# Performance work log

Measured on AMD Instinct MI355X. Metric: run time of the kernel, lower is better.

The kernel has to match this reference:

```python
import jax, jax.numpy as jnp
import numpy as np

B, D, RES, NSLOTS, NITERS = 32, 256, 64, 8, 3
NTOK = RES * RES
SCALE = D ** -0.5
EPS = 1e-8
LN_EPS = 1e-5


def _ln(x, g, b, axes=(-1,)):
    m = x.mean(axes, keepdims=True)
    v = x.var(axes, keepdims=True)
    return (x - m) / jnp.sqrt(v + LN_EPS) * g + b


def _build_grid(res):
    xy = jnp.linspace(0.0, 1.0, res)
    xx, yy = jnp.meshgrid(xy, xy, indexing='ij')
    g = jnp.stack([xx, yy], axis=-1)[None]  # [1,res,res,2]
    return jnp.concatenate([g, 1.0 - g], axis=-1)  # [1,res,res,4]


GRID = _build_grid(RES)


def setup_inputs() -> dict:
    key = jax.random.key(0)
    ks = iter(jax.random.split(key, 48))
    w = lambda shp: 0.02 * jax.random.normal(next(ks), shp, jnp.float32)
    z = lambda shp: jnp.zeros(shp, jnp.float32)
    o = lambda shp: jnp.ones(shp, jnp.float32)
    return dict(
        x=jax.random.normal(next(ks), (B, D, RES, RES), jnp.float32),
        eps_noise=jax.random.normal(next(ks), (B, NSLOTS, D), jnp.float32),
        pos_w=w((4, D)), pos_b=z((D,)),
        enc_g=o((NTOK, D)), enc_b=z((NTOK, D)),
        fm_w1=w((D, D)), fm_b1=z((D,)), fm_w2=w((D, D)), fm_b2=z((D,)),
        in_g=o((D,)), in_b=z((D,)),
        q_w=w((D, D)), q_b=z((D,)),
        k_w=w((D, D)), k_b=z((D,)),
        v_w=w((D, D)), v_b=z((D,)),
        gru_wih=w((D, 3 * D)), gru_whh=w((D, 3 * D)), gru_bih=z((3 * D,)), gru_bhh=z((3 * D,)),
        pre_g=o((D,)), pre_b=z((D,)),
        st_w1=w((D, D)), st_b1=z((D,)), st_w2=w((D, D)), st_b2=z((D,)),
        slot_g=o((D,)), slot_b=z((D,)),
        slots_loc=w((1, D)),
        slots_logscale=jax.random.uniform(next(ks), (1, D), jnp.float32),
    )


def reference(x, eps_noise, pos_w, pos_b, enc_g, enc_b, fm_w1, fm_b1, fm_w2, fm_b2,
              in_g, in_b, q_w, q_b, k_w, k_b, v_w, v_b,
              gru_wih, gru_whh, gru_bih, gru_bhh, pre_g, pre_b,
              st_w1, st_b1, st_w2, st_b2, slot_g, slot_b, slots_loc, slots_logscale):
    # SoftPositionEmbed: x + Linear(grid) permuted to NCHW
    pos = GRID @ pos_w + pos_b                       # [1,res,res,D]
    h = x + jnp.transpose(pos, (0, 3, 1, 2))         # [B,D,res,res]
    tokens = h.reshape(B, D, NTOK).transpose(0, 2, 1)  # [B,NTOK,D]
    # encoder_norm: LayerNorm over [NTOK, D] jointly
    tokens = _ln(tokens, enc_g, enc_b, axes=(-2, -1))
    tokens = jax.nn.relu(tokens @ fm_w1 + fm_b1)
    tokens = jax.nn.relu(tokens @ fm_w2 + fm_b2)
    tokens = _ln(tokens, in_g, in_b)                 # norm_input
    k = tokens @ k_w + k_b                           # [B,NTOK,D]
    v = tokens @ v_w + v_b
    # stochastic initial slots (non-variational branch)
    slots = slots_loc[None] + jnp.exp(slots_logscale)[None] * eps_noise  # [B,S,D]
    for _ in range(NITERS):
        prev = slots
        s = _ln(slots, slot_g, slot_b)               # norm_slots
        q = s @ q_w + q_b
        dots = jnp.einsum('bid,bjd->bij', q, k) * SCALE  # [B,S,NTOK]
        attn = jax.nn.softmax(dots, axis=1) + EPS    # softmax over SLOT axis
        attn = attn / attn.sum(-1, keepdims=True)    # renormalize over tokens
        upd = jnp.einsum('bij,bjd->bid', attn, v)    # [B,S,D]
        # GRUCell(update, prev) — torch gate order r,z,n
        gi = upd @ gru_wih + gru_bih
        gh = prev @ gru_whh + gru_bhh
        ir, iz, inn = jnp.split(gi, 3, axis=-1)
        hr, hz, hn = jnp.split(gh, 3, axis=-1)
        r = jax.nn.sigmoid(ir + hr)
        zt = jax.nn.sigmoid(iz + hz)
        n = jnp.tanh(inn + r * hn)
        slots = (1.0 - zt) * n + zt * prev
        # residual MLP: slots += slot_transformation(norm_pre_ff(slots))
        ff = _ln(slots, pre_g, pre_b)
        ff = jax.nn.relu(ff @ st_w1 + st_b1)
        ff = jax.nn.relu(ff @ st_w2 + st_b2)
        slots = slots + ff
    return slots
```

## Files before the change

### kernel.cpp

```cpp
#include <hip/hip_runtime.h>
#include <hip/hip_bf16.h>

typedef __attribute__((ext_vector_type(8))) short short8;
typedef __attribute__((ext_vector_type(4))) float f32x4;

#define DEVI static __device__ __forceinline__

DEVI ushort f2bf(float f) {
  union { __hip_bfloat16 h; ushort u; } c; c.h = __float2bfloat16(f); return c.u;
}
DEVI float bf2f(ushort u) {
  union { __hip_bfloat16 h; ushort u; } c; c.u = u; return __bfloat162float(c.h);
}

DEVI void gload16(const ushort* g, ushort* l) {
  __builtin_amdgcn_global_load_lds(
      (const __attribute__((address_space(1))) void*)g,
      (__attribute__((address_space(3))) void*)l, 16, 0, 0);
}

DEVI void blk_reduce2(float& a, float& b) {
  #pragma unroll
  for (int m = 1; m < 64; m <<= 1) {
    a += __shfl_xor(a, m);
    b += __shfl_xor(b, m);
  }
  __shared__ float sc[8];
  int tid = threadIdx.x, w = tid >> 6;
  if ((tid & 63) == 0) { sc[w * 2] = a; sc[w * 2 + 1] = b; }
  __syncthreads();
  if (tid == 0) {
    sc[0] = sc[0] + sc[2] + sc[4] + sc[6];
    sc[1] = sc[1] + sc[3] + sc[5] + sc[7];
  }
  __syncthreads();
  a = sc[0]; b = sc[1];
  __syncthreads();
}

DEVI void red256_2(float& a, float& b, float* sc8) {
  int tid = threadIdx.x;
  #pragma unroll
  for (int m = 1; m < 64; m <<= 1) {
    a += __shfl_xor(a, m);
    b += __shfl_xor(b, m);
  }
  if (tid < 256 && (tid & 63) == 0) { sc8[(tid >> 6) * 2] = a; sc8[(tid >> 6) * 2 + 1] = b; }
  __syncthreads();
  a = sc8[0] + sc8[2] + sc8[4] + sc8[6];
  b = sc8[1] + sc8[3] + sc8[5] + sc8[7];
  __syncthreads();
}

__global__ void kw_kernel(const float* w0, const float* w1, const float* w2, const float* w3,
                          ushort* wT, float* bstats) {
  int widx = blockIdx.y;
  const float* src = (widx == 0) ? w0 : (widx == 1) ? w1 : (widx == 2) ? w2 : w3;
  ushort* dst = wT + (size_t)widx * 65536;
  int tile = blockIdx.x;
  int k0 = (tile >> 2) * 64, n0 = (tile & 3) * 64;
  __shared__ float t[64][65];
  int tid = threadIdx.x;
  int r = tid >> 2, c0 = (tid & 3) * 16;
  #pragma unroll
  for (int j = 0; j < 16; j += 4) {
    float4 v = *reinterpret_cast<const float4*>(src + (size_t)(k0 + r) * 256 + n0 + c0 + j);
    t[r][c0 + j + 0] = v.x; t[r][c0 + j + 1] = v.y;
    t[r][c0 + j + 2] = v.z; t[r][c0 + j + 3] = v.w;
  }
  __syncthreads();
  ushort buf[16];
  #pragma unroll
  for (int j = 0; j < 16; j++) buf[j] = f2bf(t[c0 + j][r]);
  size_t o = (size_t)(n0 + r) * 256 + k0 + c0;
  *reinterpret_cast<uint4*>(dst + o) = *reinterpret_cast<uint4*>(&buf[0]);
  *reinterpret_cast<uint4*>(dst + o + 8) = *reinterpret_cast<uint4*>(&buf[8]);
  if (blockIdx.x == 0 && blockIdx.y == 0 && tid < 64) bstats[tid] = 0.f;
}

__global__ void kw2_kernel(const float* wih, const float* whh, const float* w1,
                           const float* w2, const float* qw,
                           ushort* grup, ushort* w1b, ushort* w2b, ushort* qwb) {
  int d = blockIdx.x, c = threadIdx.x;
  ushort p6[6];
  p6[0] = f2bf(wih[(size_t)d * 768 + c]);
  p6[1] = f2bf(wih[(size_t)d * 768 + 256 + c]);
  p6[2] = f2bf(wih[(size_t)d * 768 + 512 + c]);
  p6[3] = f2bf(whh[(size_t)d * 768 + c]);
  p6[4] = f2bf(whh[(size_t)d * 768 + 256 + c]);
  p6[5] = f2bf(whh[(size_t)d * 768 + 512 + c]);
  size_t o = ((size_t)d * 256 + c) * 6;
  *reinterpret_cast<uint3*>(grup + o) = *reinterpret_cast<uint3*>(p6);
  int i = d * 256 + c;
  w1b[i] = f2bf(w1[i]);
  w2b[i] = f2bf(w2[i]);
  qwb[i] = f2bf(qw[i]);
}

__global__ void k1_stats(const float* x, const float* pos_w, const float* pos_b, float* bstats) {
  int b = blockIdx.y, blk = blockIdx.x, tid = threadIdx.x;
  const float* xb = x + (size_t)b * 1048576;
  float s = 0.f, sq = 0.f;
  for (int i = 0; i < 16; i++) {
    int e4 = blk * 4096 + i * 256 + tid;
    int e = e4 * 4;
    int d = e >> 12, t = e & 4095;
    int ii = t >> 6, j0 = t & 63;
    float xx = ii * (1.f / 63.f);
    float c0 = pos_w[512 + d] + pos_w[768 + d] + pos_b[d];
    float cx = pos_w[d] - pos_w[512 + d];
    float cy = pos_w[256 + d] - pos_w[768 + d];
    float4 v = reinterpret_cast<const float4*>(xb)[e4];
    float base = c0 + xx * cx;
    #pragma unroll
    for (int j = 0; j < 4; j++) {
      float yy = (j0 + j) * (1.f / 63.f);
      float h = (&v.x)[j] + base + yy * cy;
      s += h; sq += h * h;
    }
  }
  blk_reduce2(s, sq);
  if (tid == 0) {
    atomicAdd(&bstats[b * 2], s);
    atomicAdd(&bstats[b * 2 + 1], sq);
  }
}

__global__ void k2_tokens(const float* x, const float* pos_w, const float* pos_b,
                          const float* enc_g, const float* enc_b, const float* bstats,
                          ushort* t0) {
  int tcx = blockIdx.x;
  int dcx = blockIdx.y;
  int b = blockIdx.z;
  int tid = threadIdx.x;
  float mean = bstats[b * 2] * (1.f / 1048576.f);
  float var = bstats[b * 2 + 1] * (1.f / 1048576.f) - mean * mean;
  float rstd = rsqrtf(var + 1e-5f);
  __shared__ float tt[64][65];
  const float* xb = x + (size_t)b * 1048576;
  float xx = tcx * (1.f / 63.f);
  #pragma unroll
  for (int it = 0; it < 4; it++) {
    int idx = tid + it * 256;
    int dl = idx >> 4, f4 = idx & 15;
    int d = dcx * 64 + dl;
    float c0 = pos_w[512 + d] + pos_w[768 + d] + pos_b[d];
    float cx = pos_w[d] - pos_w[512 + d];
    float cy = pos_w[256 + d] - pos_w[768 + d];
    float4 v = *reinterpret_cast<const float4*>(xb + (size_t)d * 4096 + tcx * 64 + f4 * 4);
    float base = c0 + xx * cx;
    #pragma unroll
    for (int j = 0; j < 4; j++) {
      float yy = (f4 * 4 + j) * (1.f / 63.f);
      tt[f4 * 4 + j][dl] = (&v.x)[j] + base + yy * cy;
    }
  }
  __syncthreads();
  int t_l = tid >> 2, dc = (tid & 3) * 16;
  int t = tcx * 64 + t_l;
  ushort ob[16];
  #pragma unroll
  for (int j = 0; j < 16; j++) {
    int d = dcx * 64 + dc + j;
    float h = (tt[t_l][dc + j] - mean) * rstd;
    h = h * enc_g[(size_t)t * 256 + d] + enc_b[(size_t)t * 256 + d];
    ob[j] = f2bf(h);
  }
  size_t o = (size_t)(b * 4096 + t) * 256 + dcx * 64 + dc;
  *reinterpret_cast<uint4*>(t0 + o) = *reinterpret_cast<uint4*>(&ob[0]);
  *reinterpret_cast<uint4*>(t0 + o + 8) = *reinterpret_cast<uint4*>(&ob[8]);
}

template <bool RELU, bool LN>
__global__ __launch_bounds__(512) void gemm_one(const ushort* __restrict__ A,
                                                const ushort* __restrict__ WT,
                                                const float* __restrict__ bias,
                                                const float* __restrict__ lng,
                                                const float* __restrict__ lnb,
                                                ushort* __restrict__ C) {
  __shared__ __align__(16) ushort As[128 * 64];
  __shared__ __align__(16) ushort Bs[256 * 64];
  __shared__ float rstats[128][4][2];
  int tid = threadIdx.x;
  int r0 = blockIdx.x * 128;
  int w = tid >> 6, lane = tid & 63;
  int wr = w >> 2, wc = w & 3;
  f32x4 acc[4][4];
  #pragma unroll
  for (int m = 0; m < 4; m++)
    #pragma unroll
    for (int n = 0; n < 4; n++) acc[m][n] = (f32x4)(0.f);

  for (int ks = 0; ks < 4; ks++) {
    int k0 = ks * 64;
    __syncthreads();
    #pragma unroll
    for (int i = 0; i < 2; i++) {
      int idx = tid + i * 512;
      gload16(A + (size_t)(r0 + (idx >> 3)) * 256 + k0 + (idx & 7) * 8, &As[idx * 8]);
    }
    #pragma unroll
    for (int i = 0; i < 4; i++) {
      int idx = tid + i * 512;
      gload16(WT + (size_t)(idx >> 3) * 256 + k0 + (idx & 7) * 8, &Bs[idx * 8]);
    }
    __syncthreads();
    #pragma unroll
    for (int ksub = 0; ksub < 2; ksub++) {
      int kk = ksub * 32 + (lane >> 4) * 8;
      short8 af[4], bf[4];
      #pragma unroll
      for (int m = 0; m < 4; m++)
        af[m] = *reinterpret_cast<const short8*>(&As[(wr * 64 + m * 16 + (lane & 15)) * 64 + kk]);
      #pragma unroll
      for (int n = 0; n < 4; n++)
        bf[n] = *reinterpret_cast<const short8*>(&Bs[(wc * 64 + n * 16 + (lane & 15)) * 64 + kk]);
      #pragma unroll
      for (int m = 0; m < 4; m++)
        #pragma unroll
        for (int n = 0; n < 4; n++)
          acc[m][n] = __builtin_amdgcn_mfma_f32_16x16x32_bf16(af[m], bf[n], acc[m][n], 0, 0, 0);
    }
  }
  float bcol[4], gcol[4], ocol[4];
  #pragma unroll
  for (int n = 0; n < 4; n++) {
    int col = wc * 64 + n * 16 + (lane & 15);
    bcol[n] = bias[col];
    if (LN) { gcol[n] = lng[col]; ocol[n] = lnb[col]; }
  }
  #pragma unroll
  for (int m = 0; m < 4; m++)
    #pragma unroll
    for (int n = 0; n < 4; n++)
      #pragma unroll
      for (int q = 0; q < 4; q++) {
        float v = acc[m][n][q] + bcol[n];
        if (RELU) v = fmaxf(v, 0.f);
        acc[m][n][q] = v;
      }
  if (LN) {
    #pragma unroll
    for (int m = 0; m < 4; m++)
      #pragma unroll
      for (int q = 0; q < 4; q++) {
        float rs = 0.f, rq = 0.f;
        #pragma unroll
        for (int n = 0; n < 4; n++) { float v = acc[m][n][q]; rs += v; rq += v * v; }
        #pragma unroll
        for (int msk = 1; msk < 16; msk <<= 1) { rs += __shfl_xor(rs, msk); rq += __shfl_xor(rq, msk); }
        if ((lane & 15) == 0) {
          int lr = wr * 64 + m * 16 + (lane >> 4) * 4 + q;
          rstats[lr][wc][0] = rs; rstats[lr][wc][1] = rq;
        }
      }
    __syncthreads();
    #pragma unroll
    for (int m = 0; m < 4; m++)
      #pragma unroll
      for (int q = 0; q < 4; q++) {
        int lr = wr * 64 + m * 16 + (lane >> 4) * 4 + q;
        float s = rstats[lr][0][0] + rstats[lr][1][0] + rstats[lr][2][0] + rstats[lr][3][0];
        float ssq = rstats[lr][0][1] + rstats[lr][1][1] + rstats[lr][2][1] + rstats[lr][3][1];
        float mean = s * (1.f / 256.f);
        float rstd = rsqrtf(ssq * (1.f / 256.f) - mean * mean + 1e-5f);
        #pragma unroll
        for (int n = 0; n < 4; n++)
          acc[m][n][q] = (acc[m][n][q] - mean) * rstd * gcol[n] + ocol[n];
      }
  }
  #pragma unroll
  for (int m = 0; m < 4; m++) {
    int row = r0 + wr * 64 + m * 16 + ((lane >> 4) << 2);
    #pragma unroll
    for (int n = 0; n < 4; n++) {
      int col = wc * 64 + n * 16 + (lane & 15);
      #pragma unroll
      for (int q = 0; q < 4; q++)
        C[(size_t)(row + q) * 256 + col] = f2bf(acc[m][n][q]);
    }
  }
}

__global__ __launch_bounds__(512) void gemm_kv(const ushort* __restrict__ A,
                                               const ushort* __restrict__ WTk,
                                               const ushort* __restrict__ WTv,
                                               const float* __restrict__ bk,
                                               const float* __restrict__ bv,
                                               ushort* __restrict__ Ck,
                                               ushort* __restrict__ Cv) {
  __shared__ __align__(16) ushort As[128 * 64];
  __shared__ __align__(16) ushort Bs1[256 * 64];
  __shared__ __align__(16) ushort Bs2[256 * 64];
  int tid = threadIdx.x;
  int r0 = blockIdx.x * 128;
  int w = tid >> 6, lane = tid & 63;
  int wr = w >> 2, wc = w & 3;
  f32x4 acc1[4][4], acc2[4][4];
  #pragma unroll
  for (int m = 0; m < 4; m++)
    #pragma unroll
    for (int n = 0; n < 4; n++) { acc1[m][n] = (f32x4)(0.f); acc2[m][n] = (f32x4)(0.f); }

  for (int ks = 0; ks < 4; ks++) {
    int k0 = ks * 64;
    __syncthreads();
    #pragma unroll
    for (int i = 0; i < 2; i++) {
      int idx = tid + i * 512;
      gload16(A + (size_t)(r0 + (idx >> 3)) * 256 + k0 + (idx & 7) * 8, &As[idx * 8]);
    }
    #pragma unroll
    for (int i = 0; i < 4; i++) {
      int idx = tid + i * 512;
      gload16(WTk + (size_t)(idx >> 3) * 256 + k0 + (idx & 7) * 8, &Bs1[idx * 8]);
    }
    #pragma unroll
    for (int i = 0; i < 4; i++) {
      int idx = tid + i * 512;
      gload16(WTv + (size_t)(idx >> 3) * 256 + k0 + (idx & 7) * 8, &Bs2[idx * 8]);
    }
    __syncthreads();
    #pragma unroll
    for (int ksub = 0; ksub < 2; ksub++) {
      int kk = ksub * 32 + (lane >> 4) * 8;
      short8 af[4], bf1[4], bf2[4];
      #pragma unroll
      for (int m = 0; m < 4; m++)
        af[m] = *reinterpret_cast<const short8*>(&As[(wr * 64 + m * 16 + (lane & 15)) * 64 + kk]);
      #pragma unroll
      for (int n = 0; n < 4; n++) {
        bf1[n] = *reinterpret_cast<const short8*>(&Bs1[(wc * 64 + n * 16 + (lane & 15)) * 64 + kk]);
        bf2[n] = *reinterpret_cast<const short8*>(&Bs2[(wc * 64 + n * 16 + (lane & 15)) * 64 + kk]);
      }
      #pragma unroll
      for (int m = 0; m < 4; m++)
        #pragma unroll
        for (int n = 0; n < 4; n++) {
          acc1[m][n] = __builtin_amdgcn_mfma_f32_16x16x32_bf16(af[m], bf1[n], acc1[m][n], 0, 0, 0);
          acc2[m][n] = __builtin_amdgcn_mfma_f32_16x16x32_bf16(af[m], bf2[n], acc2[m][n], 0, 0, 0);
        }
    }
  }
  #pragma unroll
  for (int m = 0; m < 4; m++) {
    int row = r0 + wr * 64 + m * 16 + ((lane >> 4) << 2);
    #pragma unroll
    for (int n = 0; n < 4; n++) {
      int col = wc * 64 + n * 16 + (lane & 15);
      float b1 = bk[col], b2 = bv[col];
      #pragma unroll
      for (int q = 0; q < 4; q++) {
        Ck[(size_t)(row + q) * 256 + col] = f2bf(acc1[m][n][q] + b1);
        Cv[(size_t)(row + q) * 256 + col] = f2bf(acc2[m][n][q] + b2);
      }
    }
  }
}

__global__ __launch_bounds__(1024) void kslots_q(const float* eps, const float* loc,
                                                 const float* lsc, const float* sg,
                                                 const float* sb, const ushort* qwb,
                                                 const float* qb, float* slots, ushort* qT,
                                                 float* upd, float* asum) {
  int s = blockIdx.x, b = blockIdx.y, tid = threadIdx.x;
  int c = tid & 255, kq = tid >> 8;
  size_t base = ((size_t)b * 8 + s) * 256;
  __shared__ float sn[256];
  __shared__ float red[4][256];
  __shared__ float sc8[8];
  float val = 0.f;
  if (tid < 256) {
    val = loc[c] + expf(lsc[c]) * eps[base + c];
    slots[base + c] = val;
    upd[base + c] = 0.f;
    qT[((size_t)b * 16 + 8 + s) * 256 + c] = 0;
    if (tid == 0) asum[b * 8 + s] = 0.f;
  }
  float aa = val, bb = val * val;
  red256_2(aa, bb, sc8);
  if (tid < 256) {
    float mean = aa * (1.f / 256.f);
    float rstd = rsqrtf(bb * (1.f / 256.f) - mean * mean + 1e-5f);
    sn[c] = (val - mean) * rstd * sg[c] + sb[c];
  }
  __syncthreads();
  float qm = 0.f;
  const ushort* qp = qwb + (size_t)(kq * 64) * 256 + c;
  #pragma unroll 8
  for (int d0 = 0; d0 < 64; d0++) qm = fmaf(sn[kq * 64 + d0], bf2f(qp[(size_t)d0 * 256]), qm);
  red[kq][c] = qm;
  __syncthreads();
  if (tid < 256) {
    float qacc = qb[c] + red[0][c] + red[1][c] + red[2][c] + red[3][c];
    qT[((size_t)b * 16 + s) * 256 + c] = f2bf(qacc * 0.0625f);
  }
}

__global__ __launch_bounds__(256) void kbc_kernel(const ushort* __restrict__ kmat,
                                                  const ushort* __restrict__ vmat,
                                                  const ushort* __restrict__ qT,
                                                  float* __restrict__ attn_sum,
                                                  float* __restrict__ upd) {
  int tcx = blockIdx.x;
  int b = blockIdx.y;
  int tid = threadIdx.x, w = tid >> 6, lane = tid & 63;
  __shared__ __align__(16) ushort Ks[256 * 64];
  __shared__ float at[256][9];
  __shared__ float wsum[4][16];
  const ushort* kbase = kmat + ((size_t)b * 4096 + tcx * 256) * 256;
  const ushort* qbase = qT + (size_t)b * 16 * 256;
  f32x4 acc[4];
  #pragma unroll
  for (int m = 0; m < 4; m++) acc[m] = (f32x4)(0.f);
  for (int ks = 0; ks < 4; ks++) {
    int k0 = ks * 64;
    __syncthreads();
    #pragma unroll
    for (int i = 0; i < 8; i++) {
      int idx = tid + i * 256;
      gload16(kbase + (size_t)(idx >> 3) * 256 + k0 + (idx & 7) * 8, &Ks[idx * 8]);
    }
    __syncthreads();
    #pragma unroll
    for (int ksub = 0; ksub < 2; ksub++) {
      int kk = ksub * 32 + (lane >> 4) * 8;
      short8 bq = *reinterpret_cast<const short8*>(qbase + (lane & 15) * 256 + k0 + kk);
      #pragma unroll
      for (int m = 0; m < 4; m++) {
        short8 af = *reinterpret_cast<const short8*>(&Ks[(w * 64 + m * 16 + (lane & 15)) * 64 + kk]);
        acc[m] = __builtin_amdgcn_mfma_f32_16x16x32_bf16(af, bq, acc[m], 0, 0, 0);
      }
    }
  }
  bool valid = (lane & 15) < 8;
  float lsum = 0.f;
  int srow = (lane >> 4) * 4;
  #pragma unroll
  for (int m = 0; m < 4; m++) {
    #pragma unroll
    for (int q = 0; q < 4; q++) {
      float d = acc[m][q];
      float mv = valid ? d : -1e30f;
      #pragma unroll
      for (int msk = 1; msk < 16; msk <<= 1) mv = fmaxf(mv, __shfl_xor(mv, msk));
      float e = valid ? expf(d - mv) : 0.f;
      float ssum = e;
      #pragma unroll
      for (int msk = 1; msk < 16; msk <<= 1) ssum += __shfl_xor(ssum, msk);
      if (valid) {
        float av = e / ssum + 1e-8f;
        int t = w * 64 + m * 16 + srow + q;
        at[t][lane & 15] = av;
        lsum += av;
      }
    }
  }
  lsum += __shfl_xor(lsum, 16);
  lsum += __shfl_xor(lsum, 32);
  if (lane < 16) wsum[w][lane] = lsum;
  __syncthreads();
  if (tid < 8) {
    float tot = wsum[0][tid] + wsum[1][tid] + wsum[2][tid] + wsum[3][tid];
    atomicAdd(&attn_sum[b * 8 + tid], tot);
  }
  float pacc[8][4];
  #pragma unroll
  for (int s = 0; s < 8; s++)
    #pragma unroll
    for (int j = 0; j < 4; j++) pacc[s][j] = 0.f;
  const ushort* vb = vmat + ((size_t)b * 4096 + tcx * 256) * 256;
  for (int ti = 0; ti < 64; ti++) {
    int t = w * 64 + ti;
    uint2 vv = *reinterpret_cast<const uint2*>(vb + (size_t)t * 256 + lane * 4);
    ushort us[4]; *reinterpret_cast<uint2*>(us) = vv;
    float vf[4];
    #pragma unroll
    for (int j = 0; j < 4; j++) vf[j] = bf2f(us[j]);
    #pragma unroll
    for (int s = 0; s < 8; s++) {
      float a = at[t][s];
      #pragma unroll
      for (int j = 0; j < 4; j++) pacc[s][j] = fmaf(a, vf[j], pacc[s][j]);
    }
  }
  float (*red)[8][256] = reinterpret_cast<float (*)[8][256]>(Ks);
  #pragma unroll
  for (int s = 0; s < 8; s++) {
    float4 v4; v4.x = pacc[s][0]; v4.y = pacc[s][1]; v4.z = pacc[s][2]; v4.w = pacc[s][3];
    *reinterpret_cast<float4*>(&red[w][s][lane * 4]) = v4;
  }
  __syncthreads();
  #pragma unroll
  for (int i = 0; i < 8; i++) {
    int idx = tid + i * 256;
    int s = idx >> 8, d = idx & 255;
    float sum = red[0][s][d] + red[1][s][d] + red[2][s][d] + red[3][s][d];
    atomicAdd(&upd[((size_t)b * 8 + s) * 256 + d], sum);
  }
}

__global__ __launch_bounds__(1024) void kd_kernel(
    const float* __restrict__ upd_in, const float* __restrict__ attn_sum,
    float* __restrict__ slots, const ushort* __restrict__ grup,
    const float* __restrict__ bih, const float* __restrict__ bhh,
    const float* __restrict__ pre_g, const float* __restrict__ pre_b,
    const ushort* __restrict__ w1b, const float* __restrict__ b1,
    const ushort* __restrict__ w2b, const float* __restrict__ b2,
    const float* __restrict__ sg, const float* __restrict__ sb,
    const ushort* __restrict__ qwb, const float* __restrict__ qb,
    ushort* __restrict__ qT_next, float* __restrict__ upd_clear,
    float* __restrict__ asum_clear, float* __restrict__ out_final) {
  int s = blockIdx.x, b = blockIdx.y;
  int tid = threadIdx.x, c = tid & 255, kq = tid >> 8;
  size_t base = ((size_t)b * 8 + s) * 256;
  __shared__ float u[256], p[256], fbuf[256];
  __shared__ float red6[6][4][256];
  __shared__ float sc8[8];
  if (tid < 256) {
    u[c] = upd_in[base + c] * (1.f / attn_sum[b * 8 + s]);
    p[c] = slots[base + c];
  }
  __syncthreads();
  float a0 = 0.f, a1 = 0.f, a2 = 0.f, a3 = 0.f, a4 = 0.f, a5 = 0.f;
  const ushort* gp = grup + ((size_t)(kq * 64) * 256 + c) * 6;
  #pragma unroll 4
  for (int d0 = 0; d0 < 64; d0++) {
    int d = kq * 64 + d0;
    uint3 w3 = *reinterpret_cast<const uint3*>(gp + (size_t)d0 * 1536);
    float ud = u[d], pd = p[d];
    a0 = fmaf(ud, bf2f((ushort)(w3.x & 0xffff)), a0);
    a1 = fmaf(ud, bf2f((ushort)(w3.x >> 16)), a1);
    a2 = fmaf(ud, bf2f((ushort)(w3.y & 0xffff)), a2);
    a3 = fmaf(pd, bf2f((ushort)(w3.y >> 16)), a3);
    a4 = fmaf(pd, bf2f((ushort)(w3.z & 0xffff)), a4);
    a5 = fmaf(pd, bf2f((ushort)(w3.z >> 16)), a5);
  }
  red6[0][kq][c] = a0; red6[1][kq][c] = a1; red6[2][kq][c] = a2;
  red6[3][kq][c] = a3; red6[4][kq][c] = a4; red6[5][kq][c] = a5;
  __syncthreads();
  float hv = 0.f;
  if (tid < 256) {
    float gi0 = bih[c], gi1 = bih[256 + c], gi2 = bih[512 + c];
    float gh0 = bhh[c], gh1 = bhh[256 + c], gh2 = bhh[512 + c];
    #pragma unroll
    for (int k2 = 0; k2 < 4; k2++) {
      gi0 += red6[0][k2][c]; gi1 += red6[1][k2][c]; gi2 += red6[2][k2][c];
      gh0 += red6[3][k2][c]; gh1 += red6[4][k2][c]; gh2 += red6[5][k2][c];
    }
    float r = 1.f / (1.f + expf(-(gi0 + gh0)));
    float z = 1.f / (1.f + expf(-(gi1 + gh1)));
    float n = tanhf(gi2 + r * gh2);
    hv = (1.f - z) * n + z * p[c];
  }
  float aa = hv, bb = hv * hv;
  red256_2(aa, bb, sc8);
  if (tid < 256) {
    float mean = aa * (1.f / 256.f);
    float rstd = rsqrtf(bb * (1.f / 256.f) - mean * mean + 1e-5f);
    fbuf[c] = (hv - mean) * rstd * pre_g[c] + pre_b[c];
  }
  __syncthreads();
  float m1 = 0.f;
  const ushort* w1p = w1b + (size_t)(kq * 64) * 256 + c;
  #pragma unroll 8
  for (int d0 = 0; d0 < 64; d0++) m1 = fmaf(fbuf[kq * 64 + d0], bf2f(w1p[(size_t)d0 * 256]), m1);
  red6[0][kq][c] = m1;
  __syncthreads();
  if (tid < 256) {
    float acc1 = b1[c] + red6[0][0][c] + red6[0][1][c] + red6[0][2][c] + red6[0][3][c];
    fbuf[c] = fmaxf(acc1, 0.f);
  }
  __syncthreads();
  float m2 = 0.f;
  const ushort* w2p = w2b + (size_t)(kq * 64) * 256 + c;
  #pragma unroll 8
  for (int d0 = 0; d0 < 64; d0++) m2 = fmaf(fbuf[kq * 64 + d0], bf2f(w2p[(size_t)d0 * 256]), m2);
  red6[1][kq][c] = m2;
  __syncthreads();
  float res = 0.f;
  if (tid < 256) {
    float acc2 = b2[c] + red6[1][0][c] + red6[1][1][c] + red6[1][2][c] + red6[1][3][c];
    res = hv + fmaxf(acc2, 0.f);
    slots[base + c] = res;
    if (qT_next == nullptr) out_final[base + c] = res;
  }
  if (qT_next != nullptr) {
    float a2s = res, b2s = res * res;
    red256_2(a2s, b2s, sc8);
    if (tid < 256) {
      float mean2 = a2s * (1.f / 256.f);
      float rstd2 = rsqrtf(b2s * (1.f / 256.f) - mean2 * mean2 + 1e-5f);
      fbuf[c] = (res - mean2) * rstd2 * sg[c] + sb[c];
    }
    __syncthreads();
    float qm = 0.f;
    const ushort* qp = qwb + (size_t)(kq * 64) * 256 + c;
    #pragma unroll 8
    for (int d0 = 0; d0 < 64; d0++) qm = fmaf(fbuf[kq * 64 + d0], bf2f(qp[(size_t)d0 * 256]), qm);
    red6[2][kq][c] = qm;
    __syncthreads();
    if (tid < 256) {
      float qacc = qb[c] + red6[2][0][c] + red6[2][1][c] + red6[2][2][c] + red6[2][3][c];
      qT_next[((size_t)b * 16 + s) * 256 + c] = f2bf(qacc * 0.0625f);
      upd_clear[base + c] = 0.f;
      if (tid == 0) asum_clear[b * 8 + s] = 0.f;
    }
  }
}

extern "C" void kernel_launch(void* const* d_in, const int* in_sizes, int n_in,
                              void* d_out, int out_size, void* d_ws, size_t ws_size,
                              hipStream_t stream) {
  const float* x         = (const float*)d_in[0];
  const float* eps_noise = (const float*)d_in[1];
  const float* pos_w     = (const float*)d_in[2];
  const float* pos_b     = (const float*)d_in[3];
  const float* enc_g     = (const float*)d_in[4];
  const float* enc_b     = (const float*)d_in[5];
  const float* fm_w1     = (const float*)d_in[6];
  const float* fm_b1     = (const float*)d_in[7];
  const float* fm_w2     = (const float*)d_in[8];
  const float* fm_b2     = (const float*)d_in[9];
  const float* in_g      = (const float*)d_in[10];
  const float* in_b      = (const float*)d_in[11];
  const float* q_w       = (const float*)d_in[12];
  const float* q_b       = (const float*)d_in[13];
  const float* k_w       = (const float*)d_in[14];
  const float* k_b       = (const float*)d_in[15];
  const float* v_w       = (const float*)d_in[16];
  const float* v_b       = (const float*)d_in[17];
  const float* gru_wih   = (const float*)d_in[18];
  const float* gru_whh   = (const float*)d_in[19];
  const float* gru_bih   = (const float*)d_in[20];
  const float* gru_bhh   = (const float*)d_in[21];
  const float* pre_g     = (const float*)d_in[22];
  const float* pre_b     = (const float*)d_in[23];
  const float* st_w1     = (const float*)d_in[24];
  const float* st_b1     = (const float*)d_in[25];
  const float* st_w2     = (const float*)d_in[26];
  const float* st_b2     = (const float*)d_in[27];
  const float* slot_g    = (const float*)d_in[28];
  const float* slot_b    = (const float*)d_in[29];
  const float* slots_loc = (const float*)d_in[30];
  const float* slots_lsc = (const float*)d_in[31];
  (void)in_sizes; (void)n_in; (void)out_size;

  char* ws = (char*)d_ws;
  const size_t OFF_BUFB   = 67108864;
  const size_t OFF_WT     = 134217728;
  const size_t OFF_QT     = OFF_WT + 524288;
  const size_t OFF_SLOTS  = OFF_QT + 262144;
  const size_t OFF_UPD    = OFF_SLOTS + 262144;
  const size_t OFF_BSTATS = OFF_UPD + 262144;
  const size_t OFF_ASUM   = OFF_BSTATS + 256;
  const size_t OFF_GRUP   = OFF_ASUM + 1024;
  const size_t OFF_W1B    = OFF_GRUP + 786432;
  const size_t OFF_W2B    = OFF_W1B + 131072;
  const size_t OFF_QWB    = OFF_W2B + 131072;
  const size_t NEED       = OFF_QWB + 131072;
  if (ws_size < NEED) return;

  ushort* bufA   = (ushort*)ws;
  ushort* bufB   = (ushort*)(ws + OFF_BUFB);
  ushort* wT     = (ushort*)(ws + OFF_WT);
  ushort* qT     = (ushort*)(ws + OFF_QT);
  float* slots   = (float*)(ws + OFF_SLOTS);
  float* upd     = (float*)(ws + OFF_UPD);
  float* bstats  = (float*)(ws + OFF_BSTATS);
  float* asum    = (float*)(ws + OFF_ASUM);
  ushort* grup   = (ushort*)(ws + OFF_GRUP);
  ushort* w1b    = (ushort*)(ws + OFF_W1B);
  ushort* w2b    = (ushort*)(ws + OFF_W2B);
  ushort* qwb    = (ushort*)(ws + OFF_QWB);

  kw_kernel<<<dim3(16, 4), 256, 0, stream>>>(fm_w1, fm_w2, k_w, v_w, wT, bstats);
  kw2_kernel<<<256, 256, 0, stream>>>(gru_wih, gru_whh, st_w1, st_w2, q_w,
                                      grup, w1b, w2b, qwb);
  k1_stats<<<dim3(64, 32), 256, 0, stream>>>(x, pos_w, pos_b, bstats);
  k2_tokens<<<dim3(64, 4, 32), 256, 0, stream>>>(x, pos_w, pos_b, enc_g, enc_b, bstats, bufA);
  gemm_one<true, false><<<1024, 512, 0, stream>>>(bufA, wT, fm_b1, nullptr, nullptr, bufA);
  gemm_one<true, true><<<1024, 512, 0, stream>>>(bufA, wT + 65536, fm_b2, in_g, in_b, bufA);
  gemm_kv<<<1024, 512, 0, stream>>>(bufA, wT + 131072, wT + 196608, k_b, v_b, bufB, bufA);
  kslots_q<<<dim3(8, 32), 1024, 0, stream>>>(eps_noise, slots_loc, slots_lsc, slot_g, slot_b,
                                             qwb, q_b, slots, qT, upd, asum);
  for (int it = 0; it < 3; it++) {
    kbc_kernel<<<dim3(16, 32), 256, 0, stream>>>(bufB, bufA, qT, asum, upd);
    bool last = (it == 2);
    kd_kernel<<<dim3(8, 32), 1024, 0, stream>>>(upd, asum, slots, grup,
        gru_bih, gru_bhh, pre_g, pre_b, w1b, st_b1, w2b, st_b2,
        slot_g, slot_b, qwb, q_b,
        last ? nullptr : qT, upd, asum, last ? (float*)d_out : nullptr);
  }
}
```

Measured before the change: 622.2 us.

## Fuse token build, feature MLP, LayerNorm and K/V projection into one kernel

Replaces the token-building kernel and three separate GEMM kernels with a single kernel that keeps a 128-token tile resident in LDS across the two MLP layers, the LayerNorm and the K/V projections. The tile uses an XOR-swizzled layout, and weights are read directly from global memory instead of being staged in LDS. Intermediate activations no longer round-trip through HBM, and three launches go away. The K-tile loads in the attention kernel also get a matching XOR swizzle to reduce LDS bank conflicts. The cost is 68KB of dynamic LDS per block, which lowers occupancy, and uncached global weight reads issued from every block.

Result: slower. 659.9 us (+6.1%).

```diff
diff --git a/kernel.cpp b/kernel.cpp
--- a/kernel.cpp
+++ b/kernel.cpp
@@ -126,95 +126,124 @@
   }
 }
 
-__global__ void k2_tokens(const float* x, const float* pos_w, const float* pos_b,
-                          const float* enc_g, const float* enc_b, const float* bstats,
-                          ushort* t0) {
-  int tcx = blockIdx.x;
-  int dcx = blockIdx.y;
-  int b = blockIdx.z;
+__global__ __launch_bounds__(512) void enc_fused(
+    const float* __restrict__ x, const float* __restrict__ pos_w,
+    const float* __restrict__ pos_b, const float* __restrict__ enc_g,
+    const float* __restrict__ enc_b, const float* __restrict__ bstats,
+    const ushort* __restrict__ WT,
+    const float* __restrict__ fb1, const float* __restrict__ fb2,
+    const float* __restrict__ lng, const float* __restrict__ lnb,
+    const float* __restrict__ kbias, const float* __restrict__ vbias,
+    ushort* __restrict__ kout, ushort* __restrict__ vout) {
+  extern __shared__ __align__(16) char smem[];
+  float (*rst)[4][2] = reinterpret_cast<float (*)[4][2]>(smem + 65536);
+  int rb = blockIdx.x, b = blockIdx.y;
   int tid = threadIdx.x;
-  float mean = bstats[b * 2] * (1.f / 1048576.f);
-  float var = bstats[b * 2 + 1] * (1.f / 1048576.f) - mean * mean;
-  float rstd = rsqrtf(var + 1e-5f);
-  __shared__ float tt[64][65];
-  const float* xb = x + (size_t)b * 1048576;
-  float xx = tcx * (1.f / 63.f);
-  #pragma unroll
-  for (int it = 0; it < 4; it++) {
-    int idx = tid + it * 256;
-    int dl = idx >> 4, f4 = idx & 15;
-    int d = dcx * 64 + dl;
-    float c0 = pos_w[512 + d] + pos_w[768 + d] + pos_b[d];
-    float cx = pos_w[d] - pos_w[512 + d];
-    float cy = pos_w[256 + d] - pos_w[768 + d];
-    float4 v = *reinterpret_cast<const float4*>(xb + (size_t)d * 4096 + tcx * 64 + f4 * 4);
-    float base = c0 + xx * cx;
-    #pragma unroll
-    for (int j = 0; j < 4; j++) {
-      float yy = (f4 * 4 + j) * (1.f / 63.f);
-      tt[f4 * 4 + j][dl] = (&v.x)[j] + base + yy * cy;
-    }
-  }
-  __syncthreads();
-  int t_l = tid >> 2, dc = (tid & 3) * 16;
-  int t = tcx * 64 + t_l;
-  ushort ob[16];
-  #pragma unroll
-  for (int j = 0; j < 16; j++) {
-    int d = dcx * 64 + dc + j;
-    float h = (tt[t_l][dc + j] - mean) * rstd;
-    h = h * enc_g[(size_t)t * 256 + d] + enc_b[(size_t)t * 256 + d];
-    ob[j] = f2bf(h);
-  }
-  size_t o = (size_t)(b * 4096 + t) * 256 + dcx * 64 + dc;
-  *reinterpret_cast<uint4*>(t0 + o) = *reinterpret_cast<uint4*>(&ob[0]);
-  *reinterpret_cast<uint4*>(t0 + o + 8) = *reinterpret_cast<uint4*>(&ob[8]);
-}
-
-template <bool RELU, bool LN>
-__global__ __launch_bounds__(512) void gemm_one(const ushort* __restrict__ A,
-                                                const ushort* __restrict__ WT,
-                                                const float* __restrict__ bias,
-                                                const float* __restrict__ lng,
-                                                const float* __restrict__ lnb,
-                                                ushort* __restrict__ C) {
-  __shared__ __align__(16) ushort As[128 * 64];
-  __shared__ __align__(16) ushort Bs[256 * 64];
-  __shared__ float rstats[128][4][2];
-  int tid = threadIdx.x;
-  int r0 = blockIdx.x * 128;
+  int t0 = rb * 128;
+
+  {
+    float mean = bstats[b * 2] * (1.f / 1048576.f);
+    float rstd = rsqrtf(bstats[b * 2 + 1] * (1.f / 1048576.f) - mean * mean + 1e-5f);
+    int tl = tid & 127, dq = tid >> 7;
+    int gt = t0 + tl;
+    float px = (float)(gt >> 6) * (1.f / 63.f), py = (float)(gt & 63) * (1.f / 63.f);
+    const float* xb = x + (size_t)b * 1048576 + gt;
+    const float* eg = enc_g + (size_t)gt * 256;
+    const float* eb = enc_b + (size_t)gt * 256;
+    #pragma unroll
+    for (int dp = 0; dp < 8; ++dp) {
+      int d0 = dq * 64 + dp * 8;
+      float4 g0 = *reinterpret_cast<const float4*>(eg + d0);
+      float4 g1 = *reinterpret_cast<const float4*>(eg + d0 + 4);
+      float4 e0 = *reinterpret_cast<const float4*>(eb + d0);
+      float4 e1 = *reinterpret_cast<const float4*>(eb + d0 + 4);
+      ushort o[8];
+      #pragma unroll
+      for (int e = 0; e < 8; ++e) {
+        int d = d0 + e;
+        float c0 = pos_w[512 + d] + pos_w[768 + d] + pos_b[d];
+        float cx = pos_w[d] - pos_w[512 + d];
+        float cy = pos_w[256 + d] - pos_w[768 + d];
+        float h = xb[(size_t)d * 4096] + c0 + px * cx + py * cy;
+        h = (h - mean) * rstd;
+        float gg = (e < 4) ? (&g0.x)[e] : (&g1.x)[e - 4];
+        float bb = (e < 4) ? (&e0.x)[e] : (&e1.x)[e - 4];
+        o[e] = f2bf(h * gg + bb);
+      }
+      *reinterpret_cast<uint4*>(smem + tl * 512 + ((d0 * 2) ^ ((tl & 7) << 4))) =
+          *reinterpret_cast<uint4*>(&o[0]);
+    }
+  }
+  __syncthreads();
+
   int w = tid >> 6, lane = tid & 63;
   int wr = w >> 2, wc = w & 3;
-  f32x4 acc[4][4];
+  int l15 = lane & 15, g = lane >> 4;
+  int col[4];
+  #pragma unroll
+  for (int n = 0; n < 4; n++) col[n] = wc * 64 + n * 16 + l15;
+
+  f32x4 acc[4][4], acc2[4][4];
+
   #pragma unroll
   for (int m = 0; m < 4; m++)
     #pragma unroll
     for (int n = 0; n < 4; n++) acc[m][n] = (f32x4)(0.f);
-
-  for (int ks = 0; ks < 4; ks++) {
-    int k0 = ks * 64;
-    __syncthreads();
-    #pragma unroll
-    for (int i = 0; i < 2; i++) {
-      int idx = tid + i * 512;
-      gload16(A + (size_t)(r0 + (idx >> 3)) * 256 + k0 + (idx & 7) * 8, &As[idx * 8]);
-    }
-    #pragma unroll
-    for (int i = 0; i < 4; i++) {
-      int idx = tid + i * 512;
-      gload16(WT + (size_t)(idx >> 3) * 256 + k0 + (idx & 7) * 8, &Bs[idx * 8]);
-    }
-    __syncthreads();
-    #pragma unroll
-    for (int ksub = 0; ksub < 2; ksub++) {
-      int kk = ksub * 32 + (lane >> 4) * 8;
+  #pragma unroll 2
+  for (int ks = 0; ks < 8; ++ks) {
+    int kb2 = ks * 64 + g * 16;
+    int ke = ks * 32 + g * 8;
+    short8 af[4], bf[4];
+    #pragma unroll
+    for (int m = 0; m < 4; m++) {
+      int r = wr * 64 + m * 16 + l15;
+      af[m] = *reinterpret_cast<const short8*>(smem + r * 512 + (kb2 ^ ((r & 7) << 4)));
+    }
+    #pragma unroll
+    for (int n = 0; n < 4; n++)
+      bf[n] = *reinterpret_cast<const short8*>(WT + (size_t)col[n] * 256 + ke);
+    #pragma unroll
+    for (int m = 0; m < 4; m++)
+      #pragma unroll
+      for (int n = 0; n < 4; n++)
+        acc[m][n] = __builtin_amdgcn_mfma_f32_16x16x32_bf16(af[m], bf[n], acc[m][n], 0, 0, 0);
+  }
+  __syncthreads();
+  #pragma unroll
+  for (int n = 0; n < 4; n++) {
+    float bv = fb1[col[n]];
+    #pragma unroll
+    for (int m = 0; m < 4; m++) {
+      int rbse = wr * 64 + m * 16 + g * 4;
+      #pragma unroll
+      for (int q = 0; q < 4; q++) {
+        int r = rbse + q;
+        float v = fmaxf(acc[m][n][q] + bv, 0.f);
+        *reinterpret_cast<ushort*>(smem + r * 512 + ((col[n] * 2) ^ ((r & 7) << 4))) = f2bf(v);
+      }
+    }
+  }
+  __syncthreads();
+
+  #pragma unroll
+  for (int m = 0; m < 4; m++)
+    #pragma unroll
+    for (int n = 0; n < 4; n++) acc[m][n] = (f32x4)(0.f);
+  {
+    const ushort* WT2 = WT + 65536;
+    #pragma unroll 2
+    for (int ks = 0; ks < 8; ++ks) {
+      int kb2 = ks * 64 + g * 16;
+      int ke = ks * 32 + g * 8;
       short8 af[4], bf[4];
       #pragma unroll
-      for (int m = 0; m < 4; m++)
-        af[m] = *reinterpret_cast<const short8*>(&As[(wr * 64 + m * 16 + (lane & 15)) * 64 + kk]);
+      for (int m = 0; m < 4; m++) {
+        int r = wr * 64 + m * 16 + l15;
+        af[m] = *reinterpret_cast<const short8*>(smem + r * 512 + (kb2 ^ ((r & 7) << 4)));
+      }
       #pragma unroll
       for (int n = 0; n < 4; n++)
-        bf[n] = *reinterpret_cast<const short8*>(&Bs[(wc * 64 + n * 16 + (lane & 15)) * 64 + kk]);
+        bf[n] = *reinterpret_cast<const short8*>(WT2 + (size_t)col[n] * 256 + ke);
       #pragma unroll
       for (int m = 0; m < 4; m++)
         #pragma unroll
@@ -222,137 +251,95 @@
           acc[m][n] = __builtin_amdgcn_mfma_f32_16x16x32_bf16(af[m], bf[n], acc[m][n], 0, 0, 0);
     }
   }
-  float bcol[4], gcol[4], ocol[4];
   #pragma unroll
   for (int n = 0; n < 4; n++) {
-    int col = wc * 64 + n * 16 + (lane & 15);
-    bcol[n] = bias[col];
-    if (LN) { gcol[n] = lng[col]; ocol[n] = lnb[col]; }
+    float bv = fb2[col[n]];
+    #pragma unroll
+    for (int m = 0; m < 4; m++)
+      #pragma unroll
+      for (int q = 0; q < 4; q++)
+        acc[m][n][q] = fmaxf(acc[m][n][q] + bv, 0.f);
   }
   #pragma unroll
   for (int m = 0; m < 4; m++)
     #pragma unroll
-    for (int n = 0; n < 4; n++)
+    for (int q = 0; q < 4; q++) {
+      float rs = 0.f, rq = 0.f;
+      #pragma unroll
+      for (int n = 0; n < 4; n++) { float v = acc[m][n][q]; rs += v; rq += v * v; }
+      #pragma unroll
+      for (int msk = 1; msk < 16; msk <<= 1) { rs += __shfl_xor(rs, msk); rq += __shfl_xor(rq, msk); }
+      if (l15 == 0) {
+        int lr = wr * 64 + m * 16 + g * 4 + q;
+        rst[lr][wc][0] = rs; rst[lr][wc][1] = rq;
+      }
+    }
+  __syncthreads();
+  {
+    float gcol[4], ocol[4];
+    #pragma unroll
+    for (int n = 0; n < 4; n++) { gcol[n] = lng[col[n]]; ocol[n] = lnb[col[n]]; }
+    #pragma unroll
+    for (int m = 0; m < 4; m++)
       #pragma unroll
       for (int q = 0; q < 4; q++) {
-        float v = acc[m][n][q] + bcol[n];
-        if (RELU) v = fmaxf(v, 0.f);
-        acc[m][n][q] = v;
-      }
-  if (LN) {
-    #pragma unroll
-    for (int m = 0; m < 4; m++)
-      #pragma unroll
-      for (int q = 0; q < 4; q++) {
-        float rs = 0.f, rq = 0.f;
-        #pragma unroll
-        for (int n = 0; n < 4; n++) { float v = acc[m][n][q]; rs += v; rq += v * v; }
-        #pragma unroll
-        for (int msk = 1; msk < 16; msk <<= 1) { rs += __shfl_xor(rs, msk); rq += __shfl_xor(rq, msk); }
-        if ((lane & 15) == 0) {
-          int lr = wr * 64 + m * 16 + (lane >> 4) * 4 + q;
-          rstats[lr][wc][0] = rs; rstats[lr][wc][1] = rq;
-        }
-      }
-    __syncthreads();
-    #pragma unroll
-    for (int m = 0; m < 4; m++)
-      #pragma unroll
-      for (int q = 0; q < 4; q++) {
-        int lr = wr * 64 + m * 16 + (lane >> 4) * 4 + q;
-        float s = rstats[lr][0][0] + rstats[lr][1][0] + rstats[lr][2][0] + rstats[lr][3][0];
-        float ssq = rstats[lr][0][1] + rstats[lr][1][1] + rstats[lr][2][1] + rstats[lr][3][1];
+        int lr = wr * 64 + m * 16 + g * 4 + q;
+        float s = rst[lr][0][0] + rst[lr][1][0] + rst[lr][2][0] + rst[lr][3][0];
+        float ssq = rst[lr][0][1] + rst[lr][1][1] + rst[lr][2][1] + rst[lr][3][1];
         float mean = s * (1.f / 256.f);
         float rstd = rsqrtf(ssq * (1.f / 256.f) - mean * mean + 1e-5f);
         #pragma unroll
-        for (int n = 0; n < 4; n++)
-          acc[m][n][q] = (acc[m][n][q] - mean) * rstd * gcol[n] + ocol[n];
-      }
-  }
-  #pragma unroll
-  for (int m = 0; m < 4; m++) {
-    int row = r0 + wr * 64 + m * 16 + ((lane >> 4) << 2);
-    #pragma unroll
-    for (int n = 0; n < 4; n++) {
-      int col = wc * 64 + n * 16 + (lane & 15);
-      #pragma unroll
-      for (int q = 0; q < 4; q++)
-        C[(size_t)(row + q) * 256 + col] = f2bf(acc[m][n][q]);
-    }
-  }
-}
-
-__global__ __launch_bounds__(512) void gemm_kv(const ushort* __restrict__ A,
-                                               const ushort* __restrict__ WTk,
-                                               const ushort* __restrict__ WTv,
-                                               const float* __restrict__ bk,
-                                               const float* __restrict__ bv,
-                                               ushort* __restrict__ Ck,
-                                               ushort* __restrict__ Cv) {
-  __shared__ __align__(16) ushort As[128 * 64];
-  __shared__ __align__(16) ushort Bs1[256 * 64];
-  __shared__ __align__(16) ushort Bs2[256 * 64];
-  int tid = threadIdx.x;
-  int r0 = blockIdx.x * 128;
-  int w = tid >> 6, lane = tid & 63;
-  int wr = w >> 2, wc = w & 3;
-  f32x4 acc1[4][4], acc2[4][4];
+        for (int n = 0; n < 4; n++) {
+          float val = (acc[m][n][q] - mean) * rstd * gcol[n] + ocol[n];
+          *reinterpret_cast<ushort*>(smem + lr * 512 + ((col[n] * 2) ^ ((lr & 7) << 4))) = f2bf(val);
+        }
+      }
+  }
+  __syncthreads();
+
   #pragma unroll
   for (int m = 0; m < 4; m++)
     #pragma unroll
-    for (int n = 0; n < 4; n++) { acc1[m][n] = (f32x4)(0.f); acc2[m][n] = (f32x4)(0.f); }
-
-  for (int ks = 0; ks < 4; ks++) {
-    int k0 = ks * 64;
-    __syncthreads();
-    #pragma unroll
-    for (int i = 0; i < 2; i++) {
-      int idx = tid + i * 512;
-      gload16(A + (size_t)(r0 + (idx >> 3)) * 256 + k0 + (idx & 7) * 8, &As[idx * 8]);
-    }
-    #pragma unroll
-    for (int i = 0; i < 4; i++) {
-      int idx = tid + i * 512;
-      gload16(WTk + (size_t)(idx >> 3) * 256 + k0 + (idx & 7) * 8, &Bs1[idx * 8]);
-    }
-    #pragma unroll
-    for (int i = 0; i < 4; i++) {
-      int idx = tid + i * 512;
-      gload16(WTv + (size_t)(idx >> 3) * 256 + k0 + (idx & 7) * 8, &Bs2[idx * 8]);
-    }
-    __syncthreads();
-    #pragma unroll
-    for (int ksub = 0; ksub < 2; ksub++) {
-      int kk = ksub * 32 + (lane >> 4) * 8;
-      short8 af[4], bf1[4], bf2[4];
-      #pragma unroll
-      for (int m = 0; m < 4; m++)
-        af[m] = *reinterpret_cast<const short8*>(&As[(wr * 64 + m * 16 + (lane & 15)) * 64 + kk]);
+    for (int n = 0; n < 4; n++) { acc[m][n] = (f32x4)(0.f); acc2[m][n] = (f32x4)(0.f); }
+  {
+    const ushort* WTk = WT + 131072;
+    const ushort* WTv = WT + 196608;
+    #pragma unroll 2
+    for (int ks = 0; ks < 8; ++ks) {
+      int kb2 = ks * 64 + g * 16;
+      int ke = ks * 32 + g * 8;
+      short8 af[4], bfk[4], bfv[4];
+      #pragma unroll
+      for (int m = 0; m < 4; m++) {
+        int r = wr * 64 + m * 16 + l15;
+        af[m] = *reinterpret_cast<const short8*>(smem + r * 512 + (kb2 ^ ((r & 7) << 4)));
+      }
       #pragma unroll
       for (int n = 0; n < 4; n++) {
-        bf1[n] = *reinterpret_cast<const short8*>(&Bs1[(wc * 64 + n * 16 + (lane & 15)) * 64 + kk]);
-        bf2[n] = *reinterpret_cast<const short8*>(&Bs2[(wc * 64 + n * 16 + (lane & 15)) * 64 + kk]);
+        bfk[n] = *reinterpret_cast<const short8*>(WTk + (size_t)col[n] * 256 + ke);
+        bfv[n] = *reinterpret_cast<const short8*>(WTv + (size_t)col[n] * 256 + ke);
       }
       #pragma unroll
       for (int m = 0; m < 4; m++)
         #pragma unroll
         for (int n = 0; n < 4; n++) {
-          acc1[m][n] = __builtin_amdgcn_mfma_f32_16x16x32_bf16(af[m], bf1[n], acc1[m][n], 0, 0, 0);
-          acc2[m][n] = __builtin_amdgcn_mfma_f32_16x16x32_bf16(af[m], bf2[n], acc2[m][n], 0, 0, 0);
+          acc[m][n] = __builtin_amdgcn_mfma_f32_16x16x32_bf16(af[m], bfk[n], acc[m][n], 0, 0, 0);
+          acc2[m][n] = __builtin_amdgcn_mfma_f32_16x16x32_bf16(af[m], bfv[n], acc2[m][n], 0, 0, 0);
         }
     }
   }
+  size_t gbase = (size_t)(b * 4096 + t0);
   #pragma unroll
   for (int m = 0; m < 4; m++) {
-    int row = r0 + wr * 64 + m * 16 + ((lane >> 4) << 2);
+    int rbse = wr * 64 + m * 16 + g * 4;
     #pragma unroll
     for (int n = 0; n < 4; n++) {
-      int col = wc * 64 + n * 16 + (lane & 15);
-      float b1 = bk[col], b2 = bv[col];
+      float kbv = kbias[col[n]], vbv = vbias[col[n]];
       #pragma unroll
       for (int q = 0; q < 4; q++) {
-        Ck[(size_t)(row + q) * 256 + col] = f2bf(acc1[m][n][q] + b1);
-        Cv[(size_t)(row + q) * 256 + col] = f2bf(acc2[m][n][q] + b2);
+        size_t o = (gbase + rbse + q) * 256 + col[n];
+        kout[o] = f2bf(acc[m][n][q] + kbv);
+        vout[o] = f2bf(acc2[m][n][q] + vbv);
       }
     }
   }
@@ -419,7 +406,8 @@
     #pragma unroll
     for (int i = 0; i < 8; i++) {
       int idx = tid + i * 256;
-      gload16(kbase + (size_t)(idx >> 3) * 256 + k0 + (idx & 7) * 8, &Ks[idx * 8]);
+      int r = idx >> 3, cc = idx & 7;
+      gload16(kbase + (size_t)r * 256 + k0 + (cc ^ (r & 7)) * 8, &Ks[idx * 8]);
     }
     __syncthreads();
     #pragma unroll
@@ -428,7 +416,9 @@
       short8 bq = *reinterpret_cast<const short8*>(qbase + (lane & 15) * 256 + k0 + kk);
       #pragma unroll
       for (int m = 0; m < 4; m++) {
-        short8 af = *reinterpret_cast<const short8*>(&Ks[(w * 64 + m * 16 + (lane & 15)) * 64 + kk]);
+        int r = w * 64 + m * 16 + (lane & 15);
+        short8 af = *reinterpret_cast<const short8*>(
+            reinterpret_cast<const char*>(Ks) + r * 128 + ((kk * 2) ^ ((r & 7) << 4)));
         acc[m] = __builtin_amdgcn_mfma_f32_16x16x32_bf16(af, bq, acc[m], 0, 0, 0);
       }
     }
@@ -674,16 +664,18 @@
   ushort* w2b    = (ushort*)(ws + OFF_W2B);
   ushort* qwb    = (ushort*)(ws + OFF_QWB);
 
+  hipFuncSetAttribute(reinterpret_cast<const void*>(enc_fused),
+                      hipFuncAttributeMaxDynamicSharedMemorySize, 69632);
+
   kw_kernel<<<dim3(16, 4), 256, 0, stream>>>(fm_w1, fm_w2, k_w, v_w, wT, bstats);
   kw2_kernel<<<256, 256, 0, stream>>>(gru_wih, gru_whh, st_w1, st_w2, q_w,
                                       grup, w1b, w2b, qwb);
   k1_stats<<<dim3(64, 32), 256, 0, stream>>>(x, pos_w, pos_b, bstats);
-  k2_tokens<<<dim3(64, 4, 32), 256, 0, stream>>>(x, pos_w, pos_b, enc_g, enc_b, bstats, bufA);
-  gemm_one<true, false><<<1024, 512, 0, stream>>>(bufA, wT, fm_b1, nullptr, nullptr, bufA);
-  gemm_one<true, true><<<1024, 512, 0, stream>>>(bufA, wT + 65536, fm_b2, in_g, in_b, bufA);
-  gemm_kv<<<1024, 512, 0, stream>>>(bufA, wT + 131072, wT + 196608, k_b, v_b, bufB, bufA);
   kslots_q<<<dim3(8, 32), 1024, 0, stream>>>(eps_noise, slots_loc, slots_lsc, slot_g, slot_b,
                                              qwb, q_b, slots, qT, upd, asum);
+  enc_fused<<<dim3(32, 32), 512, 69632, stream>>>(
+      x, pos_w, pos_b, enc_g, enc_b, bstats, wT,
+      fm_b1, fm_b2, in_g, in_b, k_b, v_b, bufB, bufA);
   for (int it = 0; it < 3; it++) {
     kbc_kernel<<<dim3(16, 32), 256, 0, stream>>>(bufB, bufA, qT, asum, upd);
     bool last = (it == 2);
```
